# Optimization experiments

Measured on AMD Instinct MI355X. Metric: run time of the kernel, lower is better.

Reference implementation:

```python
import jax, jax.numpy as jnp
import numpy as np
from jax import lax

WARMUP = 365
X1S = (100.0, 1200.0); X2S = (-5.0, 3.0); X3S = (20.0, 300.0); X4S = (1.1, 2.9)
K1, K2 = 3, 6  # max UH kernel lengths: ceil(x4_max)=3, ceil(2*x4_max)=6


def _uh_kernels(x4):
    # x4: [B]. S-curve differences, padded with zeros beyond ceil(x4)/ceil(2*x4).
    t1 = jnp.arange(K1 + 1, dtype=x4.dtype)
    sh1 = jnp.minimum(t1[None, :] / x4[:, None], 1.0) ** 2.5          # [B, K1+1]
    uh1 = sh1[:, 1:] - sh1[:, :-1]                                     # [B, K1]
    t2 = jnp.arange(K2 + 1, dtype=x4.dtype)
    r = t2[None, :] / x4[:, None]
    sh2 = jnp.where(t2[None, :] <= x4[:, None],
                    0.5 * r ** 2.5,
                    1.0 - 0.5 * jnp.maximum(2.0 - r, 0.0) ** 2.5)      # [B, K2+1]
    uh2 = sh2[:, 1:] - sh2[:, :-1]                                     # [B, K2]
    return uh1, uh2


def _causal_conv(x, uh):
    # x: [T, B], uh: [B, K] -> y[t,b] = sum_k uh[b,k] * x[t-k,b]
    T = x.shape[0]
    out = jnp.zeros_like(x)
    for k in range(uh.shape[1]):  # K is small and static (<=6)
        shifted = jnp.pad(x, ((k, 0), (0, 0)))[:T]
        out = out + uh[:, k][None, :] * shifted
    return out


def _gr4j_core(p_and_e, x1, x2, x3, x4, s0, r0):
    # p_and_e: [T, B, 2]
    diff = p_and_e[:, :, 0] - p_and_e[:, :, 1]
    pn = jnp.maximum(diff, 0.0)   # net precip [T, B]
    en = jnp.maximum(-diff, 0.0)  # net evap   [T, B]

    def prod_step(s, pe):
        p, e = pe
        s = jnp.clip(s, 0.0, x1)
        tp = jnp.tanh(p / x1)
        te = jnp.tanh(e / x1)
        ps = x1 * (1.0 - (s / x1) ** 2) * tp / (1.0 + s / x1 * tp)
        es = s * (2.0 - s / x1) * te / (1.0 + (1.0 - s / x1) * te)
        s2 = jnp.clip(s - es + ps, 0.0, x1)
        perc = s2 * (1.0 - (1.0 + (4.0 / 9.0 * s2 / x1) ** 4) ** (-0.25))
        s2 = s2 - perc
        pr = perc + (pn_step := p - ps) * 1.0 + 0.0 * pn_step  # pr = perc + (pn - ps)
        return s2, pr

    s_final, prs = lax.scan(prod_step, s0, (pn, en))  # prs: [T, B]

    uh1, uh2 = _uh_kernels(x4)
    q9 = _causal_conv(prs, uh1)  # [T, B]
    q1 = _causal_conv(prs, uh2)  # [T, B]

    def route_step(r, q):
        q9t, q1t = q
        r = jnp.clip(r, 0.0, x3)
        gex = x2 * (r / x3) ** 3.5
        r2 = jnp.maximum(0.0, r + q9t + gex)
        qr = r2 * (1.0 - (1.0 + (r2 / x3) ** 4) ** (-0.25))
        r2 = r2 - qr
        qd = jnp.maximum(0.0, q1t + gex)
        return r2, qr + qd

    r_final, q = lax.scan(route_step, r0, (q9, q1))  # q: [T, B]
    return q, s_final, r_final


def _forward(p_and_e, parameters):
    x1 = X1S[0] + parameters[:, 0] * (X1S[1] - X1S[0])
    x2 = X2S[0] + parameters[:, 1] * (X2S[1] - X2S[0])
    x3 = X3S[0] + parameters[:, 2] * (X3S[1] - X3S[0])
    x4 = X4S[0] + parameters[:, 3] * (X4S[1] - X4S[0])
    if WARMUP > 0:
        # warmup runs under no_grad in torch: stop gradients through it
        _, s_w, r_w = _gr4j_core(p_and_e[:WARMUP], x1, x2, x3, x4,
                                 0.5 * lax.stop_gradient(x1),
                                 0.5 * lax.stop_gradient(x3))
        s0 = lax.stop_gradient(s_w)
        r0 = lax.stop_gradient(r_w)
    else:
        s0 = 0.5 * lax.stop_gradient(x1)
        r0 = 0.5 * lax.stop_gradient(x3)
    q, _, _ = _gr4j_core(p_and_e[WARMUP:], x1, x2, x3, x4, s0, r0)
    return q[:, :, None]  # [T-WARMUP, B, 1]


def setup_inputs() -> dict:
    key = jax.random.key(0)
    k1, k2 = jax.random.split(key)
    p_and_e = jax.random.uniform(k1, (4015, 2048, 2), dtype=jnp.float32)
    parameters = jax.random.uniform(k2, (2048, 4), dtype=jnp.float32)
    return {"p_and_e": p_and_e, "parameters": parameters}


def reference(p_and_e, parameters):
    return _forward(p_and_e, parameters)
```

## Files before the change

### kernel.cpp

```cpp
#include <hip/hip_runtime.h>


#define T_TOTAL 4015
#define NWARM   365
#define NB      2048
#define BSTEP   55
#define NBATCH  73

__global__ __launch_bounds__(128, 1)
void gr4j_kernel(const float2* __restrict__ pe_in,
                 const float*  __restrict__ params,
                 float*        __restrict__ out)
{
    const int lane = threadIdx.x & 63;
    const int wid  = threadIdx.x >> 6;
    const int b    = blockIdx.x * 64 + lane;

    __shared__ float prbuf[2][BSTEP * 64];
    __shared__ int produced;
    __shared__ int consumed;
    if (threadIdx.x == 0) { produced = 0; consumed = 0; }
    __syncthreads();

    const float x1 = 100.0f + params[b * 4 + 0] * 1100.0f;
    const float x2 = -5.0f  + params[b * 4 + 1] * 8.0f;
    const float x3 = 20.0f  + params[b * 4 + 2] * 280.0f;
    const float x4 = 1.1f   + params[b * 4 + 3] * 1.8f;
    const float invx1 = __builtin_amdgcn_rcpf(x1);
    const float invx3 = __builtin_amdgcn_rcpf(x3);
    const float c49   = (4.0f / 9.0f) * invx1;
    const float c49_2 = c49 * c49;
    const float c4s   = c49_2 * c49_2;
    const float i3_2  = invx3 * invx3;
    const float c4r   = i3_2 * i3_2;

    if (wid == 0) {
        float s = 0.5f * x1;

        auto prod_step = [&](float2 pe) -> float {
            const float diff = pe.x - pe.y;
            const float pn = fmaxf(diff, 0.0f);
            const float en = fmaxf(-diff, 0.0f);
            const float ap = pn * invx1;
            const float ae = en * invx1;
            const float sx = s * invx1;
            const float dp = fmaf(sx, ap, 1.0f);
            const float de = fmaf(1.0f - sx, ae, 1.0f);
            const float n1 = fmaf(-sx, sx, 1.0f);
            const float nump = pn * n1;
            const float nume = (sx * en) * (2.0f - sx);
            const float rpe = __builtin_amdgcn_rcpf(dp * de);
            const float a_ = nump * de;
            const float b_ = nume * dp;
            const float s2 = fmaf(a_ - b_, rpe, s);
            const float ps = a_ * rpe;
            const float s22 = s2 * s2;
            const float s24 = s22 * s22;
            const float z = c4s * s24;
            float w = fmaf(z, 15.0f / 128.0f, -5.0f / 32.0f);
            w = fmaf(z, w, 0.25f);
            const float perc = (s2 * z) * w;
            s = s2 - perc;
            return perc + (pn - ps);
        };

        const float2* gptr = pe_in + b;
        float2 rot[11];
        #pragma unroll
        for (int i = 0; i < 11; ++i) rot[i] = gptr[(size_t)i * NB];

        for (int k = 0; k < NBATCH; ++k) {
            if (k >= 2) {
                while (__hip_atomic_load(&consumed, __ATOMIC_ACQUIRE,
                                         __HIP_MEMORY_SCOPE_WORKGROUP) < k - 1) {}
            }
            float* dst = &prbuf[k & 1][0] + lane;
            const int tb = k * BSTEP;
            const int grf = (k < NBATCH - 1) ? 5 : 4;
            for (int g = 0; g < 5; ++g) {
                float* d2 = dst + g * (11 * 64);
                if (g < grf) {
                    const float2* gp = gptr + (size_t)(tb + g * 11 + 11) * NB;
                    #pragma unroll
                    for (int i = 0; i < 11; ++i) {
                        const float2 pe = rot[i];
                        rot[i] = gp[(size_t)i * NB];
                        d2[i * 64] = prod_step(pe);
                    }
                } else {
                    #pragma unroll
                    for (int i = 0; i < 11; ++i)
                        d2[i * 64] = prod_step(rot[i]);
                }
            }
            __hip_atomic_store(&produced, k + 1, __ATOMIC_RELEASE,
                               __HIP_MEMORY_SCOPE_WORKGROUP);
        }
    } else {
        float u10, u11, u12, u20, u21, u22, u23, u24, u25;
        {
            float sh[3];
            #pragma unroll
            for (int j = 1; j <= 3; ++j)
                sh[j - 1] = powf(fminf((float)j / x4, 1.0f), 2.5f);
            u10 = sh[0]; u11 = sh[1] - sh[0]; u12 = sh[2] - sh[1];
            float s2h[6];
            #pragma unroll
            for (int j = 1; j <= 6; ++j) {
                float rr = (float)j / x4;
                s2h[j - 1] = ((float)j <= x4) ? 0.5f * powf(rr, 2.5f)
                           : 1.0f - 0.5f * powf(fmaxf(2.0f - rr, 0.0f), 2.5f);
            }
            u20 = s2h[0];          u21 = s2h[1] - s2h[0]; u22 = s2h[2] - s2h[1];
            u23 = s2h[3] - s2h[2]; u24 = s2h[4] - s2h[3]; u25 = s2h[5] - s2h[4];
        }

        float r = 0.5f * x3;
        float ph0 = 0.f, ph1 = 0.f, ph2 = 0.f, ph3 = 0.f, ph4 = 0.f;

        auto w1_step = [&](float pr) -> float {
            const float q9 = fmaf(u10, pr, fmaf(u11, ph0, u12 * ph1));
            const float q1 = fmaf(u20, pr, fmaf(u21, ph0, fmaf(u22, ph1,
                             fmaf(u23, ph2, fmaf(u24, ph3, u25 * ph4)))));
            ph4 = ph3; ph3 = ph2; ph2 = ph1; ph1 = ph0; ph0 = pr;
            const float rq = r + q9;
            const float rx = r * invx3;
            const float srx = __builtin_amdgcn_sqrtf(rx);
            const float gex = (x2 * ((rx * rx) * rx)) * srx;
            const float r2 = fmaxf(0.0f, rq + gex);
            const float r22 = r2 * r2;
            const float r24 = r22 * r22;
            const float v4p1 = fmaf(c4r, r24, 1.0f);
            const float rn = r2 * __builtin_amdgcn_rsqf(__builtin_amdgcn_sqrtf(v4p1));
            const float qr = r2 - rn;
            r = rn;
            return qr + fmaxf(0.0f, q1 + gex);
        };

        for (int k = 0; k < NBATCH; ++k) {
            while (__hip_atomic_load(&produced, __ATOMIC_ACQUIRE,
                                     __HIP_MEMORY_SCOPE_WORKGROUP) < k + 1) {}
            const float* src = &prbuf[k & 1][0] + lane;
            if (k != 6) {
                float* ob = (k < 6)
                    ? out + (size_t)(k * BSTEP) * NB + b
                    : out + (size_t)(k * BSTEP - NWARM) * NB + b;
                float prr[11];
                #pragma unroll
                for (int i = 0; i < 11; ++i) prr[i] = src[i * 64];
                for (int g = 0; g < 5; ++g) {
                    const float* sp = src + (g + 1) * (11 * 64);
                    float* ob2 = ob + (size_t)(g * 11) * NB;
                    if (g < 4) {
                        #pragma unroll
                        for (int i = 0; i < 11; ++i) {
                            const float pr = prr[i];
                            prr[i] = sp[i * 64];
                            ob2[(size_t)i * NB] = w1_step(pr);
                        }
                    } else {
                        #pragma unroll
                        for (int i = 0; i < 11; ++i)
                            ob2[(size_t)i * NB] = w1_step(prr[i]);
                    }
                }
            } else {
                float* dumpb = out + (size_t)330 * NB + b;
                float* realb = out + b;
                float prr[11];
                #pragma unroll
                for (int i = 0; i < 11; ++i) prr[i] = src[i * 64];
                #pragma unroll
                for (int g = 0; g < 5; ++g) {
                    #pragma unroll
                    for (int i = 0; i < 11; ++i) {
                        const int j = g * 11 + i;
                        const float pr = prr[i];
                        if (g < 4) prr[i] = src[(j + 11) * 64];
                        if (j == 35) { ph0 = ph1 = ph2 = ph3 = ph4 = 0.0f; }
                        const float q = w1_step(pr);
                        if (j < 35) dumpb[(size_t)j * NB] = q;
                        else        realb[(size_t)(j - 35) * NB] = q;
                    }
                }
            }
            __hip_atomic_store(&consumed, k + 1, __ATOMIC_RELEASE,
                               __HIP_MEMORY_SCOPE_WORKGROUP);
        }
    }
}

extern "C" void kernel_launch(void* const* d_in, const int* in_sizes, int n_in,
                              void* d_out, int out_size, void* d_ws, size_t ws_size,
                              hipStream_t stream) {
    const float2* pe_in  = (const float2*)d_in[0];
    const float*  params = (const float*)d_in[1];
    float* out = (float*)d_out;
    (void)in_sizes; (void)n_in; (void)out_size; (void)d_ws; (void)ws_size;

    gr4j_kernel<<<dim3(NB / 64), dim3(128), 0, stream>>>(pe_in, params, out);
}
```

Baseline: 398.2 us.

## Stream forcing inputs via global_load_lds into a 4-slot LDS ring

Replaces the register-rotation prefetch of float2 forcing data in the producer wave with direct global-to-LDS dword loads into a four-slot ring buffer, prefetching two chunks ahead and gating reads with explicit vmcnt waits. The intent is to free VGPRs and decouple memory latency from the serial production-store recurrence. It adds LDS traffic, splits each float2 load into two dword loads, and relies on hand-counted s_waitcnt values matching the compiler's outstanding load count, which is fragile.

```diff
diff --git a/kernel.cpp b/kernel.cpp
--- a/kernel.cpp
+++ b/kernel.cpp
@@ -6,6 +6,16 @@
 #define NB      2048
 #define BSTEP   55
 #define NBATCH  73
+#define CH      11
+#define NCHUNK  365
+
+typedef __attribute__((address_space(3))) float       lds_f;
+typedef __attribute__((address_space(1))) const float glb_f;
+
+__device__ __forceinline__ void gl_lds_dword(const float* g, float* l) {
+    __builtin_amdgcn_global_load_lds((glb_f*)(uintptr_t)g,
+                                     (lds_f*)(uintptr_t)l, 4, 0, 0);
+}
 
 __global__ __launch_bounds__(128, 1)
 void gr4j_kernel(const float2* __restrict__ pe_in,
@@ -17,6 +27,7 @@
     const int b    = blockIdx.x * 64 + lane;
 
     __shared__ float prbuf[2][BSTEP * 64];
+    __shared__ float inbuf[4][CH][2][64];
     __shared__ int produced;
     __shared__ int consumed;
     if (threadIdx.x == 0) { produced = 0; consumed = 0; }
@@ -37,8 +48,8 @@
     if (wid == 0) {
         float s = 0.5f * x1;
 
-        auto prod_step = [&](float2 pe) -> float {
-            const float diff = pe.x - pe.y;
+        auto prod_step = [&](float p_, float e_) -> float {
+            const float diff = p_ - e_;
             const float pn = fmaxf(diff, 0.0f);
             const float en = fmaxf(-diff, 0.0f);
             const float ap = pn * invx1;
@@ -64,37 +75,55 @@
             return perc + (pn - ps);
         };
 
-        const float2* gptr = pe_in + b;
-        float2 rot[11];
+        const float* pbase = (const float*)pe_in + 2 * b;
+
         #pragma unroll
-        for (int i = 0; i < 11; ++i) rot[i] = gptr[(size_t)i * NB];
-
-        for (int k = 0; k < NBATCH; ++k) {
-            if (k >= 2) {
+        for (int cc = 0; cc < 2; ++cc) {
+            const float* cb = pbase + (size_t)cc * CH * 2 * NB;
+            #pragma unroll
+            for (int i = 0; i < CH; ++i) {
+                gl_lds_dword(cb + (size_t)i * 2 * NB,     &inbuf[cc][i][0][0]);
+                gl_lds_dword(cb + (size_t)i * 2 * NB + 1, &inbuf[cc][i][1][0]);
+            }
+        }
+
+        for (int c = 0; c < NCHUNK; ++c) {
+            const int k  = c / 5;
+            const int ph = c - 5 * k;
+            if (ph == 0 && k >= 2) {
                 while (__hip_atomic_load(&consumed, __ATOMIC_ACQUIRE,
                                          __HIP_MEMORY_SCOPE_WORKGROUP) < k - 1) {}
             }
-            float* dst = &prbuf[k & 1][0] + lane;
-            const int tb = k * BSTEP;
-            const int grf = (k < NBATCH - 1) ? 5 : 4;
-            for (int g = 0; g < 5; ++g) {
-                float* d2 = dst + g * (11 * 64);
-                if (g < grf) {
-                    const float2* gp = gptr + (size_t)(tb + g * 11 + 11) * NB;
-                    #pragma unroll
-                    for (int i = 0; i < 11; ++i) {
-                        const float2 pe = rot[i];
-                        rot[i] = gp[(size_t)i * NB];
-                        d2[i * 64] = prod_step(pe);
-                    }
-                } else {
-                    #pragma unroll
-                    for (int i = 0; i < 11; ++i)
-                        d2[i * 64] = prod_step(rot[i]);
+
+            if (c < NCHUNK - 1) asm volatile("s_waitcnt vmcnt(22)" ::: "memory");
+            else                asm volatile("s_waitcnt vmcnt(0)"  ::: "memory");
+
+            const int slot = c & 3;
+            float pf_p[CH], pf_e[CH];
+            #pragma unroll
+            for (int i = 0; i < CH; ++i) {
+                pf_p[i] = inbuf[slot][i][0][lane];
+                pf_e[i] = inbuf[slot][i][1][lane];
+            }
+
+            if (c + 2 < NCHUNK) {
+                const float* cb = pbase + (size_t)(c + 2) * CH * 2 * NB;
+                const int s2 = (c + 2) & 3;
+                #pragma unroll
+                for (int i = 0; i < CH; ++i) {
+                    gl_lds_dword(cb + (size_t)i * 2 * NB,     &inbuf[s2][i][0][0]);
+                    gl_lds_dword(cb + (size_t)i * 2 * NB + 1, &inbuf[s2][i][1][0]);
                 }
             }
-            __hip_atomic_store(&produced, k + 1, __ATOMIC_RELEASE,
-                               __HIP_MEMORY_SCOPE_WORKGROUP);
+
+            float* dst = &prbuf[k & 1][0] + (ph * CH) * 64 + lane;
+            #pragma unroll
+            for (int i = 0; i < CH; ++i)
+                dst[i * 64] = prod_step(pf_p[i], pf_e[i]);
+
+            if (ph == 4)
+                __hip_atomic_store(&produced, k + 1, __ATOMIC_RELEASE,
+                                   __HIP_MEMORY_SCOPE_WORKGROUP);
         }
     } else {
         float u10, u11, u12, u20, u21, u22, u23, u24, u25;
```

Result: slower. 410.2 us (+3.0%).
